# Kernel tuning notes

Hardware: AMD Instinct MI355X
Metric: run time of the kernel (lower is better)

The kernel has to match this reference:

```python
import jax, jax.numpy as jnp
import numpy as np

# Config matching init_kwargs
DILATED = (1, 2, 3)
K = 4            # proto_size
P = 96           # num_prototypes
NUM_CLASSES = 2
E = 1024         # enc_size (bert-large)
EPS = 1e-8       # torch F.cosine_similarity eps
NUM_FILTERS = (32, 32, 32)  # P // len(DILATED) per dilation


def _neg_cosine_dist(batch, p_flat, d):
    """Replicates F.unfold(kernel=(K,1), dilation=d) + view(N,1,H,K*E) + -cosine_similarity.

    batch:  (N, S, E)
    p_flat: (n, K*E) -- protolayer slice flattened exactly as torch .view does
    returns (N, n, H) with H = S - d*(K-1)
    """
    N, S, _ = batch.shape
    H = S - d * (K - 1)
    # torch unfold output is (N, K, H*E) with element [n,k,h*E+e] = batch[n, h+k*d, e];
    # the subsequent .view(N,1,H,K*E) row-major reinterprets (K,H,E) -> (H, K*E).
    x = jnp.stack([batch[:, k * d:k * d + H, :] for k in range(K)], axis=1)  # (N, K, H, E)
    x = x.reshape(N, H, K * E)  # identical flattening to torch view
    dot = jnp.einsum('nhm,pm->nph', x, p_flat)              # (N, n, H)
    xn = jnp.maximum(jnp.linalg.norm(x, axis=-1), EPS)      # (N, H)
    pn = jnp.maximum(jnp.linalg.norm(p_flat, axis=-1), EPS)  # (n,)
    cos = dot / (xn[:, None, :] * pn[None, :, None])
    return -cos


def setup_inputs() -> dict:
    key = jax.random.key(0)
    k1, k2, k3 = jax.random.split(key, 3)
    N, S = 16, 512
    embedding = jax.random.normal(k1, (N, S, E), dtype=jnp.float32)
    mask = jnp.ones((N, S), dtype=jnp.int64)
    # nn.init.uniform_ default range [0, 1)
    protolayer = jax.random.uniform(k2, (P, E, K), dtype=jnp.float32)
    fc_w = jax.random.normal(k3, (NUM_CLASSES, P), dtype=jnp.float32) * 0.1
    return {"embedding": embedding, "mask": mask, "protolayer": protolayer, "fc_w": fc_w}


def reference(embedding, mask, protolayer, fc_w):
    # protolayer (P, E, K) -> (P, K*E) exactly as torch .view(1, P, 1, K*E)
    p_flat = protolayer.reshape(P, K * E)
    dists = []
    j = 0
    for d, n in zip(DILATED, NUM_FILTERS):
        dists.append(_neg_cosine_dist(embedding, p_flat[j:j + n], d))
        j += n
    # min-pool over sliding-window positions, concat over prototype groups
    prototype_distances = jnp.concatenate([jnp.min(x, axis=2) for x in dists], axis=1)  # (N, P)
    class_out = prototype_distances @ fc_w.T  # Linear(bias=False)
    return prototype_distances, class_out
```

## Files before the change

### kernel.cpp

```cpp
#include <hip/hip_runtime.h>
#include <stdint.h>

#define EE 1024
#define SS 512
#define NBATCH 16
#define PP 96
#define NROWS (NBATCH * SS)
#define NJ (PP * 4)
#define EPS 1e-8f

typedef __attribute__((ext_vector_type(8))) short bf16x8;
typedef __attribute__((ext_vector_type(4))) float f32x4;

__device__ __forceinline__ ushort f2bf(float f) {
    uint32_t u = __float_as_uint(f);
    u += 0x7fffu + ((u >> 16) & 1u);
    return (ushort)(u >> 16);
}

__device__ __forceinline__ void gload16(const void* g, void* l) {
    __builtin_amdgcn_global_load_lds(
        (const __attribute__((address_space(1))) uint32_t*)g,
        (__attribute__((address_space(3))) uint32_t*)l, 16, 0, 0);
}

__global__ __launch_bounds__(256) void conv_kernel(const float* __restrict__ emb,
                                                   const float* __restrict__ proto,
                                                   ushort* __restrict__ ebf,
                                                   ushort* __restrict__ pbf,
                                                   float* __restrict__ rn2,
                                                   float* __restrict__ pn,
                                                   float* __restrict__ cls) {
    int b = blockIdx.x, t = threadIdx.x;
    if (b < NROWS / 4) {
        int r = b * 4 + (t >> 6);
        int l = t & 63;
        const float4* src = (const float4*)(emb + (size_t)r * EE);
        ushort4* dst = (ushort4*)(ebf + (size_t)r * EE);
        float s = 0.f;
#pragma unroll
        for (int i = 0; i < 4; i++) {
            float4 v = src[l + 64 * i];
            dst[l + 64 * i] = make_ushort4(f2bf(v.x), f2bf(v.y), f2bf(v.z), f2bf(v.w));
            s += v.x * v.x + v.y * v.y + v.z * v.z + v.w * v.w;
        }
#pragma unroll
        for (int off = 32; off; off >>= 1) s += __shfl_down(s, off);
        if (l == 0) rn2[r] = s;
    } else {
        int p = b - NROWS / 4;
        if (p == 0 && t < NBATCH * 2) cls[t] = 0.f;
        const float4* src = (const float4*)(proto + (size_t)p * 4096);
        ushort4* dst = (ushort4*)(pbf + (size_t)p * 4096);
        float s = 0.f;
#pragma unroll
        for (int i = 0; i < 4; i++) {
            float4 v = src[t + 256 * i];
            dst[t + 256 * i] = make_ushort4(f2bf(v.x), f2bf(v.y), f2bf(v.z), f2bf(v.w));
            s += v.x * v.x + v.y * v.y + v.z * v.z + v.w * v.w;
        }
#pragma unroll
        for (int off = 32; off; off >>= 1) s += __shfl_down(s, off);
        __shared__ float red[4];
        if ((t & 63) == 0) red[t >> 6] = s;
        __syncthreads();
        if (t == 0) pn[p] = sqrtf(red[0] + red[1] + red[2] + red[3]);
    }
}

#define GBM 128
#define GBN 128
#define GBK 32
#define NSPLIT 2

__global__ __launch_bounds__(256) void gemm_kernel(const ushort* __restrict__ A,
                                                   const ushort* __restrict__ B,
                                                   float* __restrict__ Rt) {
    __shared__ ushort As[GBM * GBK];
    __shared__ ushort Bs[GBN * GBK];
    int bid = blockIdx.x;
    int swz = (bid & 7) * 48 + (bid >> 3);
    int split = swz / 192;
    int rem = swz - split * 192;
    int bm = rem & 63;
    int bn = rem >> 6;
    const int klen = EE / NSPLIT;
    int kb = split * klen;
    int r0 = bm * GBM, j0 = bn * GBN;
    int tid = threadIdx.x;
    int lane = tid & 63;

    int srow = tid >> 2;
    int schunk = (tid & 3) ^ (srow & 3);
    const ushort* ga = A + (size_t)(r0 + srow) * EE + kb + schunk * 8;
    const ushort* gb = B + (size_t)(j0 + srow) * EE + kb + schunk * 8;
    ushort* lA = As + tid * 8;
    ushort* lB = Bs + tid * 8;

    int w = tid >> 6;
    int wm = (w >> 1) * 64, wn = (w & 1) * 64;
    int kc = lane >> 4;
    int fr = lane & 15;
    int fchunk = kc ^ (fr & 3);

    f32x4 acc[4][4] = {};

    for (int k0 = 0; k0 < klen; k0 += GBK) {
        __syncthreads();
        gload16(ga + k0, lA);
        gload16(ga + 64 * EE + k0, lA + 2048);
        gload16(gb + k0, lB);
        gload16(gb + 64 * EE + k0, lB + 2048);
        __syncthreads();
        bf16x8 af[4], bfr[4];
#pragma unroll
        for (int m = 0; m < 4; m++)
            af[m] = *(const bf16x8*)(As + (wm + m * 16 + fr) * GBK + fchunk * 8);
#pragma unroll
        for (int n = 0; n < 4; n++)
            bfr[n] = *(const bf16x8*)(Bs + (wn + n * 16 + fr) * GBK + fchunk * 8);
#pragma unroll
        for (int m = 0; m < 4; m++)
#pragma unroll
            for (int n = 0; n < 4; n++)
                acc[m][n] = __builtin_amdgcn_mfma_f32_16x16x32_bf16(af[m], bfr[n], acc[m][n], 0, 0, 0);
    }

    float* Rbase = Rt + (size_t)split * NJ * NROWS;
    int rloc = r0 + wm + (lane >> 4) * 4;
    int jloc = j0 + wn + fr;
#pragma unroll
    for (int m = 0; m < 4; m++)
#pragma unroll
        for (int n = 0; n < 4; n++)
            *(f32x4*)(Rbase + (size_t)(jloc + n * 16) * NROWS + rloc + m * 16) = acc[m][n];
}

#define CPAD 520

__global__ __launch_bounds__(256) void combine_kernel(const float* __restrict__ Rt,
                                                      const float* __restrict__ rn2,
                                                      const float* __restrict__ pn,
                                                      const float* __restrict__ fcw,
                                                      float* __restrict__ out,
                                                      float* __restrict__ cls) {
    __shared__ float sR[4][4][CPAD];
    __shared__ float sN2[512];
    int b = blockIdx.x;
    int n = b & 15;
    int pg = b >> 4;
    int t = threadIdx.x;
    int w = t >> 6, l = t & 63;
    int p = pg * 4 + w;

    sN2[t] = rn2[n * SS + t];
    sN2[t + 256] = rn2[n * SS + t + 256];

#pragma unroll
    for (int j = 0; j < 4; j++) {
        const float4* r0 = (const float4*)(Rt + (size_t)(4 * p + j) * NROWS + n * SS);
        const float4* r1 = (const float4*)(Rt + (size_t)(NJ + 4 * p + j) * NROWS + n * SS);
        float4 a0 = r0[l], a1 = r0[l + 64];
        float4 b0 = r1[l], b1 = r1[l + 64];
        *(float4*)&sR[w][j][4 * l] =
            make_float4(a0.x + b0.x, a0.y + b0.y, a0.z + b0.z, a0.w + b0.w);
        *(float4*)&sR[w][j][256 + 4 * l] =
            make_float4(a1.x + b1.x, a1.y + b1.y, a1.z + b1.z, a1.w + b1.w);
    }
    __syncthreads();

    int d = (p >> 5) + 1;
    int H = SS - 3 * d;
    int Hd = H - d;
    float pnv = fmaxf(pn[p], EPS);
    float best = -3.4e38f;
    for (int h = l; h < H; h += 64) {
        float dot = 0.f, x2 = 0.f;
#pragma unroll
        for (int j = 0; j < 4; j++) {
            int q = h * 4 + j;
            int k = (q >= H) + (q >= 2 * H) + (q >= 3 * H);
            int s = q - k * Hd;
            dot += sR[w][j][s];
            x2 += sN2[s];
        }
        float xn = fmaxf(sqrtf(x2), EPS);
        best = fmaxf(best, dot / (xn * pnv));
    }
#pragma unroll
    for (int off = 32; off; off >>= 1) best = fmaxf(best, __shfl_down(best, off));
    if (l == 0) {
        float pdv = -best;
        out[n * PP + p] = pdv;
        atomicAdd(&cls[n * 2 + 0], pdv * fcw[p]);
        atomicAdd(&cls[n * 2 + 1], pdv * fcw[PP + p]);
    }
}

extern "C" void kernel_launch(void* const* d_in, const int* in_sizes, int n_in,
                              void* d_out, int out_size, void* d_ws, size_t ws_size,
                              hipStream_t stream) {
    const float* emb = (const float*)d_in[0];
    const float* proto = (const float*)d_in[2];
    const float* fcw = (const float*)d_in[3];
    float* out = (float*)d_out;
    float* cls = out + NBATCH * PP;

    uint8_t* ws = (uint8_t*)d_ws;
    ushort* ebf = (ushort*)ws;
    ushort* pbf = (ushort*)(ws + (size_t)NROWS * EE * 2);
    float* rn2 = (float*)(ws + (size_t)NROWS * EE * 2 + (size_t)NJ * EE * 2);
    float* pn = rn2 + NROWS;
    float* Rt = pn + 128;

    conv_kernel<<<NROWS / 4 + PP, 256, 0, stream>>>(emb, proto, ebf, pbf, rn2, pn, cls);
    gemm_kernel<<<192 * NSPLIT, 256, 0, stream>>>(ebf, pbf, Rt);
    combine_kernel<<<NBATCH * PP / 4, 256, 0, stream>>>(Rt, rn2, pn, fcw, out, cls);
}
```

Before: 59.95 us.

## Double-buffer GEMM LDS tiles and raise split-K to four

```diff
diff --git a/kernel.cpp b/kernel.cpp
--- a/kernel.cpp
+++ b/kernel.cpp
@@ -71,21 +71,21 @@
 #define GBM 128
 #define GBN 128
 #define GBK 32
-#define NSPLIT 2
-
-__global__ __launch_bounds__(256) void gemm_kernel(const ushort* __restrict__ A,
-                                                   const ushort* __restrict__ B,
-                                                   float* __restrict__ Rt) {
-    __shared__ ushort As[GBM * GBK];
-    __shared__ ushort Bs[GBN * GBK];
+#define NSPLIT 4
+#define KLEN (EE / NSPLIT)
+#define NT (KLEN / GBK)
+
+__global__ __launch_bounds__(256, 3) void gemm_kernel(const ushort* __restrict__ A,
+                                                      const ushort* __restrict__ B,
+                                                      float* __restrict__ Rt) {
+    __shared__ ushort As[2][GBM * GBK];
+    __shared__ ushort Bs[2][GBN * GBK];
     int bid = blockIdx.x;
-    int swz = (bid & 7) * 48 + (bid >> 3);
-    int split = swz / 192;
-    int rem = swz - split * 192;
+    int split = bid / 192;
+    int rem = bid - split * 192;
     int bm = rem & 63;
     int bn = rem >> 6;
-    const int klen = EE / NSPLIT;
-    int kb = split * klen;
+    int kb = split * KLEN;
     int r0 = bm * GBM, j0 = bn * GBN;
     int tid = threadIdx.x;
     int lane = tid & 63;
@@ -94,8 +94,6 @@
     int schunk = (tid & 3) ^ (srow & 3);
     const ushort* ga = A + (size_t)(r0 + srow) * EE + kb + schunk * 8;
     const ushort* gb = B + (size_t)(j0 + srow) * EE + kb + schunk * 8;
-    ushort* lA = As + tid * 8;
-    ushort* lB = Bs + tid * 8;
 
     int w = tid >> 6;
     int wm = (w >> 1) * 64, wn = (w & 1) * 64;
@@ -105,25 +103,38 @@
 
     f32x4 acc[4][4] = {};
 
-    for (int k0 = 0; k0 < klen; k0 += GBK) {
-        __syncthreads();
-        gload16(ga + k0, lA);
-        gload16(ga + 64 * EE + k0, lA + 2048);
-        gload16(gb + k0, lB);
-        gload16(gb + 64 * EE + k0, lB + 2048);
-        __syncthreads();
+    gload16(ga, &As[0][tid * 8]);
+    gload16(ga + 64 * EE, &As[0][tid * 8 + 2048]);
+    gload16(gb, &Bs[0][tid * 8]);
+    gload16(gb + 64 * EE, &Bs[0][tid * 8 + 2048]);
+    __syncthreads();
+
+#pragma unroll
+    for (int t = 0; t < NT; ++t) {
+        int cur = t & 1;
+        if (t + 1 < NT) {
+            int k0 = (t + 1) * GBK;
+            int nb = cur ^ 1;
+            gload16(ga + k0, &As[nb][tid * 8]);
+            gload16(ga + 64 * EE + k0, &As[nb][tid * 8 + 2048]);
+            gload16(gb + k0, &Bs[nb][tid * 8]);
+            gload16(gb + 64 * EE + k0, &Bs[nb][tid * 8 + 2048]);
+        }
+        const ushort* as = As[cur];
+        const ushort* bs = Bs[cur];
         bf16x8 af[4], bfr[4];
 #pragma unroll
         for (int m = 0; m < 4; m++)
-            af[m] = *(const bf16x8*)(As + (wm + m * 16 + fr) * GBK + fchunk * 8);
+            af[m] = *(const bf16x8*)(as + (wm + m * 16 + fr) * GBK + fchunk * 8);
 #pragma unroll
         for (int n = 0; n < 4; n++)
-            bfr[n] = *(const bf16x8*)(Bs + (wn + n * 16 + fr) * GBK + fchunk * 8);
+            bfr[n] = *(const bf16x8*)(bs + (wn + n * 16 + fr) * GBK + fchunk * 8);
 #pragma unroll
         for (int m = 0; m < 4; m++)
 #pragma unroll
             for (int n = 0; n < 4; n++)
                 acc[m][n] = __builtin_amdgcn_mfma_f32_16x16x32_bf16(af[m], bfr[n], acc[m][n], 0, 0, 0);
+        __syncthreads();
     }
 
     float* Rbase = Rt + (size_t)split * NJ * NROWS;
@@ -158,14 +169,17 @@
 
 #pragma unroll
     for (int j = 0; j < 4; j++) {
-        const float4* r0 = (const float4*)(Rt + (size_t)(4 * p + j) * NROWS + n * SS);
-        const float4* r1 = (const float4*)(Rt + (size_t)(NJ + 4 * p + j) * NROWS + n * SS);
-        float4 a0 = r0[l], a1 = r0[l + 64];
-        float4 b0 = r1[l], b1 = r1[l + 64];
-        *(float4*)&sR[w][j][4 * l] =
-            make_float4(a0.x + b0.x, a0.y + b0.y, a0.z + b0.z, a0.w + b0.w);
-        *(float4*)&sR[w][j][256 + 4 * l] =
-            make_float4(a1.x + b1.x, a1.y + b1.y, a1.z + b1.z, a1.w + b1.w);
+        float4 s0 = make_float4(0.f, 0.f, 0.f, 0.f);
+        float4 s1 = make_float4(0.f, 0.f, 0.f, 0.f);
+#pragma unroll
+        for (int pl = 0; pl < NSPLIT; pl++) {
+            const float4* rp = (const float4*)(Rt + ((size_t)pl * NJ + 4 * p + j) * NROWS + n * SS);
+            float4 a0 = rp[l], a1 = rp[l + 64];
+            s0.x += a0.x; s0.y += a0.y; s0.z += a0.z; s0.w += a0.w;
+            s1.x += a1.x; s1.y += a1.y; s1.z += a1.z; s1.w += a1.w;
+        }
+        *(float4*)&sR[w][j][4 * l] = s0;
+        *(float4*)&sR[w][j][256 + 4 * l] = s1;
     }
     __syncthreads();
 
```

Result: no change. 59.27 us (-1.1%).

## Restructure GEMM to full-N 32-row tiles with double-buffered LDS, drop split-K

Applied to the files above, without the earlier changes.

```diff
diff --git a/kernel.cpp b/kernel.cpp
--- a/kernel.cpp
+++ b/kernel.cpp
@@ -68,72 +68,82 @@
     }
 }
 
-#define GBM 128
-#define GBN 128
+#define BROWS 32
 #define GBK 32
-#define NSPLIT 2
-
-__global__ __launch_bounds__(256) void gemm_kernel(const ushort* __restrict__ A,
-                                                   const ushort* __restrict__ B,
-                                                   float* __restrict__ Rt) {
-    __shared__ ushort As[GBM * GBK];
-    __shared__ ushort Bs[GBN * GBK];
-    int bid = blockIdx.x;
-    int swz = (bid & 7) * 48 + (bid >> 3);
-    int split = swz / 192;
-    int rem = swz - split * 192;
-    int bm = rem & 63;
-    int bn = rem >> 6;
-    const int klen = EE / NSPLIT;
-    int kb = split * klen;
-    int r0 = bm * GBM, j0 = bn * GBN;
-    int tid = threadIdx.x;
-    int lane = tid & 63;
-
-    int srow = tid >> 2;
-    int schunk = (tid & 3) ^ (srow & 3);
-    const ushort* ga = A + (size_t)(r0 + srow) * EE + kb + schunk * 8;
-    const ushort* gb = B + (size_t)(j0 + srow) * EE + kb + schunk * 8;
-    ushort* lA = As + tid * 8;
-    ushort* lB = Bs + tid * 8;
-
-    int w = tid >> 6;
-    int wm = (w >> 1) * 64, wn = (w & 1) * 64;
+#define NKT (EE / GBK)
+#define BCH (NJ * GBK / 8)
+#define ACH (BROWS * GBK / 8)
+
+__global__ __launch_bounds__(512, 2) void gemm_kernel(const ushort* __restrict__ A,
+                                                      const ushort* __restrict__ B,
+                                                      float* __restrict__ Rt) {
+    __shared__ ushort As[2][BROWS * GBK];
+    __shared__ ushort Bs[2][NJ * GBK];
+    int r0 = blockIdx.x * BROWS;
+    int t = threadIdx.x;
+    int lane = t & 63;
+    int w = t >> 6;
+    int fr = lane & 15;
     int kc = lane >> 4;
-    int fr = lane & 15;
-    int fchunk = kc ^ (fr & 3);
-
-    f32x4 acc[4][4] = {};
-
-    for (int k0 = 0; k0 < klen; k0 += GBK) {
+
+    int cB0 = t;
+    int rB0 = cB0 >> 2;     int gB0 = (cB0 & 3) ^ (rB0 & 3);
+    int cB1 = t + 512;      int rB1 = cB1 >> 2;  int gB1 = (cB1 & 3) ^ (rB1 & 3);
+    int cB2 = t + 1024;     int rB2 = cB2 >> 2;  int gB2 = (cB2 & 3) ^ (rB2 & 3);
+    int rA = t >> 2;        int gA = (t & 3) ^ (rA & 3);
+    const ushort* gb0 = B + (size_t)rB0 * EE + gB0 * 8;
+    const ushort* gb1 = B + (size_t)rB1 * EE + gB1 * 8;
+    const ushort* gb2 = B + (size_t)rB2 * EE + gB2 * 8;
+    const ushort* ga = A + (size_t)(r0 + rA) * EE + gA * 8;
+
+    f32x4 acc[2][3] = {};
+
+    gload16(gb0, &Bs[0][cB0 * 8]);
+    gload16(gb1, &Bs[0][cB1 * 8]);
+    gload16(gb2, &Bs[0][cB2 * 8]);
+    if (t < ACH) gload16(ga, &As[0][t * 8]);
+    __syncthreads();
+
+#pragma unroll 4
+    for (int tt = 0; tt < NKT; ++tt) {
+        int cur = tt & 1;
+        if (tt + 1 < NKT) {
+            int k0 = (tt + 1) * GBK;
+            int nb = cur ^ 1;
+            gload16(gb0 + k0, &Bs[nb][cB0 * 8]);
+            gload16(gb1 + k0, &Bs[nb][cB1 * 8]);
+            gload16(gb2 + k0, &Bs[nb][cB2 * 8]);
+            if (t < ACH) gload16(ga + k0, &As[nb][t * 8]);
+        }
+        const ushort* as = As[cur];
+        const ushort* bs = Bs[cur];
+        bf16x8 af[2], bf[3];
+#pragma unroll
+        for (int m = 0; m < 2; m++) {
+            int row = m * 16 + fr;
+            af[m] = *(const bf16x8*)(as + row * GBK + (kc ^ (row & 3)) * 8);
+        }
+#pragma unroll
+        for (int n = 0; n < 3; n++) {
+            int row = w * 48 + n * 16 + fr;
+            bf[n] = *(const bf16x8*)(bs + row * GBK + (kc ^ (row & 3)) * 8);
+        }
+#pragma unroll
+        for (int m = 0; m < 2; m++)
+#pragma unroll
+            for (int n = 0; n < 3; n++)
+                acc[m][n] = __builtin_amdgcn_mfma_f32_16x16x32_bf16(af[m], bf[n], acc[m][n], 0, 0, 0);
         __syncthreads();
-        gload16(ga + k0, lA);
-        gload16(ga + 64 * EE + k0, lA + 2048);
-        gload16(gb + k0, lB);
-        gload16(gb + 64 * EE + k0, lB + 2048);
-        __syncthreads();
-        bf16x8 af[4], bfr[4];
-#pragma unroll
-        for (int m = 0; m < 4; m++)
-            af[m] = *(const bf16x8*)(As + (wm + m * 16 + fr) * GBK + fchunk * 8);
-#pragma unroll
-        for (int n = 0; n < 4; n++)
-            bfr[n] = *(const bf16x8*)(Bs + (wn + n * 16 + fr) * GBK + fchunk * 8);
-#pragma unroll
-        for (int m = 0; m < 4; m++)
-#pragma unroll
-            for (int n = 0; n < 4; n++)
-                acc[m][n] = __builtin_amdgcn_mfma_f32_16x16x32_bf16(af[m], bfr[n], acc[m][n], 0, 0, 0);
-    }
-
-    float* Rbase = Rt + (size_t)split * NJ * NROWS;
-    int rloc = r0 + wm + (lane >> 4) * 4;
-    int jloc = j0 + wn + fr;
-#pragma unroll
-    for (int m = 0; m < 4; m++)
-#pragma unroll
-        for (int n = 0; n < 4; n++)
-            *(f32x4*)(Rbase + (size_t)(jloc + n * 16) * NROWS + rloc + m * 16) = acc[m][n];
+    }
+
+    int rloc = r0 + (lane >> 4) * 4;
+#pragma unroll
+    for (int m = 0; m < 2; m++)
+#pragma unroll
+        for (int n = 0; n < 3; n++) {
+            int jloc = w * 48 + n * 16 + fr;
+            *(f32x4*)(Rt + (size_t)jloc * NROWS + rloc + m * 16) = acc[m][n];
+        }
 }
 
 #define CPAD 520
@@ -158,14 +168,9 @@
 
 #pragma unroll
     for (int j = 0; j < 4; j++) {
-        const float4* r0 = (const float4*)(Rt + (size_t)(4 * p + j) * NROWS + n * SS);
-        const float4* r1 = (const float4*)(Rt + (size_t)(NJ + 4 * p + j) * NROWS + n * SS);
-        float4 a0 = r0[l], a1 = r0[l + 64];
-        float4 b0 = r1[l], b1 = r1[l + 64];
-        *(float4*)&sR[w][j][4 * l] =
-            make_float4(a0.x + b0.x, a0.y + b0.y, a0.z + b0.z, a0.w + b0.w);
-        *(float4*)&sR[w][j][256 + 4 * l] =
-            make_float4(a1.x + b1.x, a1.y + b1.y, a1.z + b1.z, a1.w + b1.w);
+        const float4* rp = (const float4*)(Rt + (size_t)(4 * p + j) * NROWS + n * SS);
+        *(float4*)&sR[w][j][4 * l] = rp[l];
+        *(float4*)&sR[w][j][256 + 4 * l] = rp[l + 64];
     }
     __syncthreads();
 
@@ -214,6 +219,6 @@
     float* Rt = pn + 128;
 
     conv_kernel<<<NROWS / 4 + PP, 256, 0, stream>>>(emb, proto, ebf, pbf, rn2, pn, cls);
-    gemm_kernel<<<192 * NSPLIT, 256, 0, stream>>>(ebf, pbf, Rt);
+    gemm_kernel<<<NROWS / BROWS, 512, 0, stream>>>(ebf, pbf, Rt);
     combine_kernel<<<NBATCH * PP / 4, 256, 0, stream>>>(Rt, rn2, pn, fcw, out, cls);
 }
```

Result: slower. 64.57 us (+7.7%).
